# Performance work log

Hardware: AMD Instinct MI355X
Metric: run time of the kernel (lower is better)

Reference implementation:

```python
import jax, jax.numpy as jnp
import numpy as np

N = 10000
E = 320000
D_IN = 256
D_HID = 256
D_OUT = 256


def setup_inputs() -> dict:
    key = jax.random.key(0)
    ks = jax.random.split(key, 6)
    x = jax.random.normal(ks[0], (N, D_IN), dtype=jnp.float32)
    edge_index = jax.random.randint(ks[1], (2, E), 0, N, dtype=jnp.int64)
    s1 = 1.0 / np.sqrt(D_IN)
    s2 = 1.0 / np.sqrt(D_HID)
    W1 = jax.random.uniform(ks[2], (D_IN, D_HID), jnp.float32, -s1, s1)
    b1 = jax.random.uniform(ks[3], (D_HID,), jnp.float32, -s1, s1)
    W2 = jax.random.uniform(ks[4], (D_HID, D_OUT), jnp.float32, -s2, s2)
    b2 = jax.random.uniform(ks[5], (D_OUT,), jnp.float32, -s2, s2)
    return {"x": x, "edge_index": edge_index, "W1": W1, "b1": b1, "W2": W2, "b2": b2}


def reference(x, edge_index, W1, b1, W2, b2):
    # GINConv with default eps=0: h_i = (1+eps)*x_i + sum_{(j->i) in E} x_j
    src = edge_index[0]
    dst = edge_index[1]
    agg = jax.ops.segment_sum(x[src], dst, num_segments=N)  # [N, D_IN]
    h = x + agg  # eps = 0
    # 2-layer MLP: Linear -> ReLU -> Linear
    h = jax.nn.relu(jnp.dot(h, W1) + b1)
    return jnp.dot(h, W2) + b2
```

## Files before the change

kernel.cpp:

```cpp
#include <hip/hip_runtime.h>

#define NN 10000
#define EE 320000
#define DD 256
#define CAP 96
#define POISON 0xAAAAAAAAu

typedef __attribute__((ext_vector_type(8))) short short8;
typedef __attribute__((ext_vector_type(4))) float f32x4;

__device__ __forceinline__ float bf_lo(unsigned u) { return __uint_as_float(u << 16); }
__device__ __forceinline__ float bf_hi(unsigned u) { return __uint_as_float(u & 0xffff0000u); }
__device__ __forceinline__ unsigned short f2bf(float f) {
    unsigned u = __float_as_uint(f);
    u += 0x7fffu + ((u >> 16) & 1u);
    return (unsigned short)(u >> 16);
}

__global__ __launch_bounds__(256) void prep_kernel(
    const float* __restrict__ x, unsigned short* __restrict__ xb,
    const float* __restrict__ W1, const float* __restrict__ W2,
    unsigned short* __restrict__ W1t, unsigned short* __restrict__ W2t,
    const int* __restrict__ src, const int* __restrict__ dst,
    int* __restrict__ counts, int* __restrict__ slots)
{
    __shared__ float tile[64][65];
    const int bid = blockIdx.x;
    const int tid = threadIdx.x;
    if (bid < 1250) {
        const int i = bid * 2048 + tid * 8;
        const float4 a = *(const float4*)(x + i);
        const float4 b = *(const float4*)(x + i + 4);
        unsigned short o[8] = {f2bf(a.x), f2bf(a.y), f2bf(a.z), f2bf(a.w),
                               f2bf(b.x), f2bf(b.y), f2bf(b.z), f2bf(b.w)};
        *(short8*)(xb + i) = *(short8*)o;
    } else if (bid < 1282) {
        int wid = bid - 1250;
        const float* W = (wid & 16) ? W2 : W1;
        unsigned short* Wt = (wid & 16) ? W2t : W1t;
        wid &= 15;
        const int k0 = (wid & 3) * 64, n0 = (wid >> 2) * 64;
        const int tx = tid & 63, ty = tid >> 6;
        for (int r = ty; r < 64; r += 4)
            tile[r][tx] = W[(size_t)(k0 + r) * 256 + n0 + tx];
        __syncthreads();
        for (int r = ty; r < 64; r += 4)
            Wt[(size_t)(n0 + r) * 256 + k0 + tx] = f2bf(tile[tx][r]);
    } else {
        const int e = (bid - 1282) * 256 + tid;
        const int d = dst[e];
        const int s = src[e];
        const unsigned rank = (unsigned)atomicAdd(&counts[d], 1) - POISON;
        if (rank < CAP) slots[d * CAP + rank] = s;
    }
}

__global__ __launch_bounds__(256) void gather_kernel(
    const unsigned short* __restrict__ xb,
    const int* __restrict__ counts,
    const int* __restrict__ slots,
    unsigned short* __restrict__ aggb)
{
    const int wave = (int)((blockIdx.x * blockDim.x + threadIdx.x) >> 6);
    const int lane = threadIdx.x & 63;
    if (wave >= NN) return;
    int deg = (int)((unsigned)counts[wave] - POISON);
    deg = min(max(deg, 0), CAP);
    const int* sl = slots + wave * CAP;
    const uint4* xv = (const uint4*)xb;

    const int half = lane >> 5;
    const int sub  = lane & 31;

    float acc[8];
    {
        const uint4 self = xv[(size_t)wave * 32 + sub];
        const unsigned w[4] = {self.x, self.y, self.z, self.w};
#pragma unroll
        for (int q = 0; q < 4; ++q) {
            acc[2 * q]     = half ? 0.f : bf_lo(w[q]);
            acc[2 * q + 1] = half ? 0.f : bf_hi(w[q]);
        }
    }

    int j = 0;
    for (; j + 7 < deg; j += 8) {
        uint4 v[4];
#pragma unroll
        for (int u = 0; u < 4; ++u)
            v[u] = xv[(size_t)sl[j + 2 * u + half] * 32 + sub];
#pragma unroll
        for (int u = 0; u < 4; ++u) {
            const unsigned w[4] = {v[u].x, v[u].y, v[u].z, v[u].w};
#pragma unroll
            for (int q = 0; q < 4; ++q) {
                acc[2 * q]     += bf_lo(w[q]);
                acc[2 * q + 1] += bf_hi(w[q]);
            }
        }
    }
    for (; j < deg; j += 2) {
        const int k = j + half;
        const bool valid = (k < deg);
        const int n = valid ? sl[k] : wave;
        uint4 v = xv[(size_t)n * 32 + sub];
        if (!valid) { v.x = 0; v.y = 0; v.z = 0; v.w = 0; }
        const unsigned w[4] = {v.x, v.y, v.z, v.w};
#pragma unroll
        for (int q = 0; q < 4; ++q) {
            acc[2 * q]     += bf_lo(w[q]);
            acc[2 * q + 1] += bf_hi(w[q]);
        }
    }

#pragma unroll
    for (int q = 0; q < 8; ++q)
        acc[q] += __shfl_xor(acc[q], 32, 64);

    if (half == 0) {
        unsigned o[4];
#pragma unroll
        for (int q = 0; q < 4; ++q)
            o[q] = (unsigned)f2bf(acc[2 * q]) | ((unsigned)f2bf(acc[2 * q + 1]) << 16);
        ((uint4*)aggb)[(size_t)wave * 32 + sub] = make_uint4(o[0], o[1], o[2], o[3]);
    }
}

__global__ __launch_bounds__(256) void mlp_kernel(
    const unsigned short* __restrict__ aggb,
    const unsigned short* __restrict__ W1t,
    const unsigned short* __restrict__ W2t,
    const float* __restrict__ b1,
    const float* __restrict__ b2,
    float* __restrict__ out, int M)
{
    __shared__ unsigned short h1[32][264];
    const int tid = threadIdx.x;
    const int wv = tid >> 6, lane = tid & 63;
    const int quad = lane >> 4, l16 = lane & 15;
    const int m0 = blockIdx.x * 32;
    const int n0 = wv * 64;

    int rowA0 = m0 + l16;       if (rowA0 > M - 1) rowA0 = M - 1;
    int rowA1 = m0 + 16 + l16;  if (rowA1 > M - 1) rowA1 = M - 1;
    const short* Ap  = (const short*)aggb;
    const short* W1p = (const short*)W1t;
    const short* W2p = (const short*)W2t;

    f32x4 acc[2][4] = {};
#pragma unroll
    for (int kk = 0; kk < 256; kk += 32) {
        const int ko = kk + quad * 8;
        const short8 a0 = *(const short8*)(Ap + (size_t)rowA0 * 256 + ko);
        const short8 a1 = *(const short8*)(Ap + (size_t)rowA1 * 256 + ko);
#pragma unroll
        for (int j = 0; j < 4; ++j) {
            const short8 b = *(const short8*)(W1p + (size_t)(n0 + j * 16 + l16) * 256 + ko);
            acc[0][j] = __builtin_amdgcn_mfma_f32_16x16x32_bf16(a0, b, acc[0][j], 0, 0, 0);
            acc[1][j] = __builtin_amdgcn_mfma_f32_16x16x32_bf16(a1, b, acc[1][j], 0, 0, 0);
        }
    }
#pragma unroll
    for (int j = 0; j < 4; ++j) {
        const int col = n0 + j * 16 + l16;
        const float bs = b1[col];
#pragma unroll
        for (int mi = 0; mi < 2; ++mi)
#pragma unroll
            for (int r = 0; r < 4; ++r) {
                const int row = mi * 16 + quad * 4 + r;
                h1[row][col] = f2bf(fmaxf(acc[mi][j][r] + bs, 0.f));
            }
    }
    __syncthreads();

    f32x4 acc2[2][4] = {};
#pragma unroll
    for (int kk = 0; kk < 256; kk += 32) {
        const int ko = kk + quad * 8;
        const short8 a0 = *(const short8*)&h1[l16][ko];
        const short8 a1 = *(const short8*)&h1[16 + l16][ko];
#pragma unroll
        for (int j = 0; j < 4; ++j) {
            const short8 b = *(const short8*)(W2p + (size_t)(n0 + j * 16 + l16) * 256 + ko);
            acc2[0][j] = __builtin_amdgcn_mfma_f32_16x16x32_bf16(a0, b, acc2[0][j], 0, 0, 0);
            acc2[1][j] = __builtin_amdgcn_mfma_f32_16x16x32_bf16(a1, b, acc2[1][j], 0, 0, 0);
        }
    }
#pragma unroll
    for (int j = 0; j < 4; ++j) {
        const int col = n0 + j * 16 + l16;
        const float bs = b2[col];
#pragma unroll
        for (int mi = 0; mi < 2; ++mi)
#pragma unroll
            for (int r = 0; r < 4; ++r) {
                const int row = m0 + mi * 16 + quad * 4 + r;
                if (row < M)
                    out[(size_t)row * 256 + col] = acc2[mi][j][r] + bs;
            }
    }
}

extern "C" void kernel_launch(void* const* d_in, const int* in_sizes, int n_in,
                              void* d_out, int out_size, void* d_ws, size_t ws_size,
                              hipStream_t stream)
{
    const float* x   = (const float*)d_in[0];
    const int*   ei  = (const int*)d_in[1];
    const float* W1  = (const float*)d_in[2];
    const float* b1  = (const float*)d_in[3];
    const float* W2  = (const float*)d_in[4];
    const float* b2  = (const float*)d_in[5];
    float* out = (float*)d_out;

    const int E = in_sizes[1] / 2;
    const int* src = ei;
    const int* dst = ei + E;

    unsigned short* xb   = (unsigned short*)d_ws;
    unsigned short* aggb = xb + (size_t)NN * DD;
    unsigned short* W1t  = aggb + (size_t)NN * DD;
    unsigned short* W2t  = W1t + 256 * 256;
    int* counts = (int*)(W2t + 256 * 256);
    int* slots  = counts + NN;

    prep_kernel<<<2532, 256, 0, stream>>>(x, xb, W1, W2, W1t, W2t,
                                          src, dst, counts, slots);
    gather_kernel<<<(NN + 3) / 4, 256, 0, stream>>>(xb, counts, slots, aggb);
    mlp_kernel<<<(NN + 31) / 32, 256, 0, stream>>>(aggb, W1t, W2t, b1, b2, out, NN);

    (void)E; (void)ws_size; (void)n_in; (void)out_size;
}
```

Baseline: 134.7 us.

## Split gather across feature quarters, use 16-bit slot indices, enlarge MLP row tile

```diff
diff --git a/kernel.cpp b/kernel.cpp
--- a/kernel.cpp
+++ b/kernel.cpp
@@ -22,7 +22,7 @@
     const float* __restrict__ W1, const float* __restrict__ W2,
     unsigned short* __restrict__ W1t, unsigned short* __restrict__ W2t,
     const int* __restrict__ src, const int* __restrict__ dst,
-    int* __restrict__ counts, int* __restrict__ slots)
+    int* __restrict__ counts, unsigned short* __restrict__ slots)
 {
     __shared__ float tile[64][65];
     const int bid = blockIdx.x;
@@ -51,78 +51,80 @@
         const int d = dst[e];
         const int s = src[e];
         const unsigned rank = (unsigned)atomicAdd(&counts[d], 1) - POISON;
-        if (rank < CAP) slots[d * CAP + rank] = s;
+        if (rank < CAP) slots[(size_t)d * CAP + rank] = (unsigned short)s;
     }
 }
 
 __global__ __launch_bounds__(256) void gather_kernel(
     const unsigned short* __restrict__ xb,
     const int* __restrict__ counts,
-    const int* __restrict__ slots,
+    const unsigned short* __restrict__ slots,
     unsigned short* __restrict__ aggb)
 {
-    const int wave = (int)((blockIdx.x * blockDim.x + threadIdx.x) >> 6);
+    const int bid = blockIdx.x;
+    const int q = bid / 2500;
+    const int node = (bid - q * 2500) * 4 + (threadIdx.x >> 6);
     const int lane = threadIdx.x & 63;
-    if (wave >= NN) return;
-    int deg = (int)((unsigned)counts[wave] - POISON);
+    const int grp = lane >> 3, sub = lane & 7;
+    const int qoff = q * 8 + sub;
+
+    int deg = (int)((unsigned)counts[node] - POISON);
     deg = min(max(deg, 0), CAP);
-    const int* sl = slots + wave * CAP;
+    const unsigned short* sl = slots + (size_t)node * CAP;
     const uint4* xv = (const uint4*)xb;
-
-    const int half = lane >> 5;
-    const int sub  = lane & 31;
 
     float acc[8];
     {
-        const uint4 self = xv[(size_t)wave * 32 + sub];
+        const uint4 self = xv[(size_t)node * 32 + qoff];
         const unsigned w[4] = {self.x, self.y, self.z, self.w};
 #pragma unroll
-        for (int q = 0; q < 4; ++q) {
-            acc[2 * q]     = half ? 0.f : bf_lo(w[q]);
-            acc[2 * q + 1] = half ? 0.f : bf_hi(w[q]);
+        for (int t = 0; t < 4; ++t) {
+            acc[2 * t]     = grp ? 0.f : bf_lo(w[t]);
+            acc[2 * t + 1] = grp ? 0.f : bf_hi(w[t]);
         }
     }
 
+#define ACC4(v) { \
+        acc[0] += bf_lo((v).x); acc[1] += bf_hi((v).x); \
+        acc[2] += bf_lo((v).y); acc[3] += bf_hi((v).y); \
+        acc[4] += bf_lo((v).z); acc[5] += bf_hi((v).z); \
+        acc[6] += bf_lo((v).w); acc[7] += bf_hi((v).w); }
+
     int j = 0;
-    for (; j + 7 < deg; j += 8) {
-        uint4 v[4];
-#pragma unroll
-        for (int u = 0; u < 4; ++u)
-            v[u] = xv[(size_t)sl[j + 2 * u + half] * 32 + sub];
-#pragma unroll
-        for (int u = 0; u < 4; ++u) {
-            const unsigned w[4] = {v[u].x, v[u].y, v[u].z, v[u].w};
-#pragma unroll
-            for (int q = 0; q < 4; ++q) {
-                acc[2 * q]     += bf_lo(w[q]);
-                acc[2 * q + 1] += bf_hi(w[q]);
-            }
-        }
-    }
-    for (; j < deg; j += 2) {
-        const int k = j + half;
-        const bool valid = (k < deg);
-        const int n = valid ? sl[k] : wave;
-        uint4 v = xv[(size_t)n * 32 + sub];
+    for (; j + 16 <= deg; j += 16) {
+        const int s0 = (int)sl[j + grp];
+        const int s1 = (int)sl[j + 8 + grp];
+        const uint4 v0 = xv[(size_t)s0 * 32 + qoff];
+        const uint4 v1 = xv[(size_t)s1 * 32 + qoff];
+        ACC4(v0); ACC4(v1);
+    }
+    for (; j + 8 <= deg; j += 8) {
+        const int s0 = (int)sl[j + grp];
+        const uint4 v0 = xv[(size_t)s0 * 32 + qoff];
+        ACC4(v0);
+    }
+    if (j < deg) {
+        const int k = j + grp;
+        const bool valid = k < deg;
+        const int s0 = valid ? (int)sl[k] : node;
+        uint4 v = xv[(size_t)s0 * 32 + qoff];
         if (!valid) { v.x = 0; v.y = 0; v.z = 0; v.w = 0; }
-        const unsigned w[4] = {v.x, v.y, v.z, v.w};
-#pragma unroll
-        for (int q = 0; q < 4; ++q) {
-            acc[2 * q]     += bf_lo(w[q]);
-            acc[2 * q + 1] += bf_hi(w[q]);
-        }
-    }
-
-#pragma unroll
-    for (int q = 0; q < 8; ++q)
-        acc[q] += __shfl_xor(acc[q], 32, 64);
-
-    if (half == 0) {
+        ACC4(v);
+    }
+#undef ACC4
+
+#pragma unroll
+    for (int m = 8; m <= 32; m <<= 1)
+#pragma unroll
+        for (int t = 0; t < 8; ++t)
+            acc[t] += __shfl_xor(acc[t], m, 64);
+
+    if (grp == 0) {
         unsigned o[4];
 #pragma unroll
-        for (int q = 0; q < 4; ++q)
-            o[q] = (unsigned)f2bf(acc[2 * q]) | ((unsigned)f2bf(acc[2 * q + 1]) << 16);
-        ((uint4*)aggb)[(size_t)wave * 32 + sub] = make_uint4(o[0], o[1], o[2], o[3]);
+        for (int t = 0; t < 4; ++t)
+            o[t] = (unsigned)f2bf(acc[2 * t]) | ((unsigned)f2bf(acc[2 * t + 1]) << 16);
+        ((uint4*)aggb)[(size_t)node * 32 + qoff] = make_uint4(o[0], o[1], o[2], o[3]);
     }
 }
 
@@ -134,30 +136,37 @@
     const float* __restrict__ b2,
     float* __restrict__ out, int M)
 {
-    __shared__ unsigned short h1[32][264];
+    __shared__ unsigned short h1[48][264];
     const int tid = threadIdx.x;
     const int wv = tid >> 6, lane = tid & 63;
     const int quad = lane >> 4, l16 = lane & 15;
-    const int m0 = blockIdx.x * 32;
+    const int m0 = blockIdx.x * 48;
     const int n0 = wv * 64;
 
-    int rowA0 = m0 + l16;       if (rowA0 > M - 1) rowA0 = M - 1;
-    int rowA1 = m0 + 16 + l16;  if (rowA1 > M - 1) rowA1 = M - 1;
+    int rows[3];
+#pragma unroll
+    for (int mi = 0; mi < 3; ++mi) {
+        int r = m0 + mi * 16 + l16;
+        rows[mi] = r < M ? r : M - 1;
+    }
     const short* Ap  = (const short*)aggb;
     const short* W1p = (const short*)W1t;
     const short* W2p = (const short*)W2t;
 
-    f32x4 acc[2][4] = {};
+    f32x4 acc[3][4] = {};
 #pragma unroll
     for (int kk = 0; kk < 256; kk += 32) {
         const int ko = kk + quad * 8;
-        const short8 a0 = *(const short8*)(Ap + (size_t)rowA0 * 256 + ko);
-        const short8 a1 = *(const short8*)(Ap + (size_t)rowA1 * 256 + ko);
+        short8 a[3];
+#pragma unroll
+        for (int mi = 0; mi < 3; ++mi)
+            a[mi] = *(const short8*)(Ap + (size_t)rows[mi] * 256 + ko);
 #pragma unroll
         for (int j = 0; j < 4; ++j) {
             const short8 b = *(const short8*)(W1p + (size_t)(n0 + j * 16 + l16) * 256 + ko);
-            acc[0][j] = __builtin_amdgcn_mfma_f32_16x16x32_bf16(a0, b, acc[0][j], 0, 0, 0);
-            acc[1][j] = __builtin_amdgcn_mfma_f32_16x16x32_bf16(a1, b, acc[1][j], 0, 0, 0);
+#pragma unroll
+            for (int mi = 0; mi < 3; ++mi)
+                acc[mi][j] = __builtin_amdgcn_mfma_f32_16x16x32_bf16(a[mi], b, acc[mi][j], 0, 0, 0);
         }
     }
 #pragma unroll
@@ -165,7 +174,7 @@
         const int col = n0 + j * 16 + l16;
         const float bs = b1[col];
 #pragma unroll
-        for (int mi = 0; mi < 2; ++mi)
+        for (int mi = 0; mi < 3; ++mi)
 #pragma unroll
             for (int r = 0; r < 4; ++r) {
                 const int row = mi * 16 + quad * 4 + r;
@@ -174,17 +183,20 @@
     }
     __syncthreads();
 
-    f32x4 acc2[2][4] = {};
+    f32x4 acc2[3][4] = {};
 #pragma unroll
     for (int kk = 0; kk < 256; kk += 32) {
         const int ko = kk + quad * 8;
-        const short8 a0 = *(const short8*)&h1[l16][ko];
-        const short8 a1 = *(const short8*)&h1[16 + l16][ko];
+        short8 a[3];
+#pragma unroll
+        for (int mi = 0; mi < 3; ++mi)
+            a[mi] = *(const short8*)&h1[mi * 16 + l16][ko];
 #pragma unroll
         for (int j = 0; j < 4; ++j) {
             const short8 b = *(const short8*)(W2p + (size_t)(n0 + j * 16 + l16) * 256 + ko);
-            acc2[0][j] = __builtin_amdgcn_mfma_f32_16x16x32_bf16(a0, b, acc2[0][j], 0, 0, 0);
-            acc2[1][j] = __builtin_amdgcn_mfma_f32_16x16x32_bf16(a1, b, acc2[1][j], 0, 0, 0);
+#pragma unroll
+            for (int mi = 0; mi < 3; ++mi)
+                acc2[mi][j] = __builtin_amdgcn_mfma_f32_16x16x32_bf16(a[mi], b, acc2[mi][j], 0, 0, 0);
         }
     }
 #pragma unroll
@@ -192,7 +204,7 @@
         const int col = n0 + j * 16 + l16;
         const float bs = b2[col];
 #pragma unroll
-        for (int mi = 0; mi < 2; ++mi)
+        for (int mi = 0; mi < 3; ++mi)
 #pragma unroll
             for (int r = 0; r < 4; ++r) {
                 const int row = m0 + mi * 16 + quad * 4 + r;
@@ -223,12 +235,12 @@
     unsigned short* W1t  = aggb + (size_t)NN * DD;
     unsigned short* W2t  = W1t + 256 * 256;
     int* counts = (int*)(W2t + 256 * 256);
-    int* slots  = counts + NN;
+    unsigned short* slots = (unsigned short*)(counts + NN);
 
     prep_kernel<<<2532, 256, 0, stream>>>(x, xb, W1, W2, W1t, W2t,
                                           src, dst, counts, slots);
-    gather_kernel<<<(NN + 3) / 4, 256, 0, stream>>>(xb, counts, slots, aggb);
-    mlp_kernel<<<(NN + 31) / 32, 256, 0, stream>>>(aggb, W1t, W2t, b1, b2, out, NN);
+    gather_kernel<<<NN, 256, 0, stream>>>(xb, counts, slots, aggb);
+    mlp_kernel<<<(NN + 47) / 48, 256, 0, stream>>>(aggb, W1t, W2t, b1, b2, out, NN);
 
     (void)E; (void)ws_size; (void)n_in; (void)out_size;
 }
```

After: 132.2 us. No clear change (-1.9%).

## Fuse neighbor gather into MLP kernel and store slot indices as 16-bit

Applied to the files above, without the earlier changes.

```diff
diff --git a/kernel.cpp b/kernel.cpp
--- a/kernel.cpp
+++ b/kernel.cpp
@@ -22,7 +22,7 @@
     const float* __restrict__ W1, const float* __restrict__ W2,
     unsigned short* __restrict__ W1t, unsigned short* __restrict__ W2t,
     const int* __restrict__ src, const int* __restrict__ dst,
-    int* __restrict__ counts, int* __restrict__ slots)
+    int* __restrict__ counts, unsigned short* __restrict__ slots)
 {
     __shared__ float tile[64][65];
     const int bid = blockIdx.x;
@@ -51,140 +51,134 @@
         const int d = dst[e];
         const int s = src[e];
         const unsigned rank = (unsigned)atomicAdd(&counts[d], 1) - POISON;
-        if (rank < CAP) slots[d * CAP + rank] = s;
-    }
-}
-
-__global__ __launch_bounds__(256) void gather_kernel(
+        if (rank < CAP) slots[(size_t)d * CAP + rank] = (unsigned short)s;
+    }
+}
+
+__global__ __launch_bounds__(512, 4) void gather_mlp_kernel(
     const unsigned short* __restrict__ xb,
     const int* __restrict__ counts,
-    const int* __restrict__ slots,
-    unsigned short* __restrict__ aggb)
-{
-    const int wave = (int)((blockIdx.x * blockDim.x + threadIdx.x) >> 6);
-    const int lane = threadIdx.x & 63;
-    if (wave >= NN) return;
-    int deg = (int)((unsigned)counts[wave] - POISON);
-    deg = min(max(deg, 0), CAP);
-    const int* sl = slots + wave * CAP;
-    const uint4* xv = (const uint4*)xb;
-
-    const int half = lane >> 5;
-    const int sub  = lane & 31;
-
-    float acc[8];
-    {
-        const uint4 self = xv[(size_t)wave * 32 + sub];
-        const unsigned w[4] = {self.x, self.y, self.z, self.w};
-#pragma unroll
-        for (int q = 0; q < 4; ++q) {
-            acc[2 * q]     = half ? 0.f : bf_lo(w[q]);
-            acc[2 * q + 1] = half ? 0.f : bf_hi(w[q]);
-        }
-    }
-
-    int j = 0;
-    for (; j + 7 < deg; j += 8) {
-        uint4 v[4];
-#pragma unroll
-        for (int u = 0; u < 4; ++u)
-            v[u] = xv[(size_t)sl[j + 2 * u + half] * 32 + sub];
-#pragma unroll
-        for (int u = 0; u < 4; ++u) {
-            const unsigned w[4] = {v[u].x, v[u].y, v[u].z, v[u].w};
-#pragma unroll
-            for (int q = 0; q < 4; ++q) {
-                acc[2 * q]     += bf_lo(w[q]);
-                acc[2 * q + 1] += bf_hi(w[q]);
-            }
-        }
-    }
-    for (; j < deg; j += 2) {
-        const int k = j + half;
-        const bool valid = (k < deg);
-        const int n = valid ? sl[k] : wave;
-        uint4 v = xv[(size_t)n * 32 + sub];
-        if (!valid) { v.x = 0; v.y = 0; v.z = 0; v.w = 0; }
-        const unsigned w[4] = {v.x, v.y, v.z, v.w};
-#pragma unroll
-        for (int q = 0; q < 4; ++q) {
-            acc[2 * q]     += bf_lo(w[q]);
-            acc[2 * q + 1] += bf_hi(w[q]);
-        }
-    }
-
-#pragma unroll
-    for (int q = 0; q < 8; ++q)
-        acc[q] += __shfl_xor(acc[q], 32, 64);
-
-    if (half == 0) {
-        unsigned o[4];
-#pragma unroll
-        for (int q = 0; q < 4; ++q)
-            o[q] = (unsigned)f2bf(acc[2 * q]) | ((unsigned)f2bf(acc[2 * q + 1]) << 16);
-        ((uint4*)aggb)[(size_t)wave * 32 + sub] = make_uint4(o[0], o[1], o[2], o[3]);
-    }
-}
-
-__global__ __launch_bounds__(256) void mlp_kernel(
-    const unsigned short* __restrict__ aggb,
+    const unsigned short* __restrict__ slots,
     const unsigned short* __restrict__ W1t,
     const unsigned short* __restrict__ W2t,
     const float* __restrict__ b1,
     const float* __restrict__ b2,
     float* __restrict__ out, int M)
 {
-    __shared__ unsigned short h1[32][264];
+    __shared__ unsigned short buf[32][264];
     const int tid = threadIdx.x;
-    const int wv = tid >> 6, lane = tid & 63;
+    const int wave = tid >> 6, lane = tid & 63;
+    const int m0 = blockIdx.x * 32;
+
+    {
+        const int half = lane >> 5;
+        const int sub  = lane & 31;
+        const uint4* xv = (const uint4*)xb;
+
+        for (int rr = 0; rr < 4; ++rr) {
+            const int r = wave * 4 + rr;
+            int node = m0 + r; if (node > M - 1) node = M - 1;
+            int deg = (int)((unsigned)counts[node] - POISON);
+            deg = min(max(deg, 0), CAP);
+            const unsigned short* sl = slots + (size_t)node * CAP;
+
+            float acc[8];
+            {
+                const uint4 self = xv[(size_t)node * 32 + sub];
+                const unsigned w[4] = {self.x, self.y, self.z, self.w};
+#pragma unroll
+                for (int q = 0; q < 4; ++q) {
+                    acc[2 * q]     = half ? 0.f : bf_lo(w[q]);
+                    acc[2 * q + 1] = half ? 0.f : bf_hi(w[q]);
+                }
+            }
+
+            int j = 0;
+            for (; j + 7 < deg; j += 8) {
+                uint4 v[4];
+#pragma unroll
+                for (int u = 0; u < 4; ++u)
+                    v[u] = xv[(size_t)sl[j + 2 * u + half] * 32 + sub];
+#pragma unroll
+                for (int u = 0; u < 4; ++u) {
+                    const unsigned w[4] = {v[u].x, v[u].y, v[u].z, v[u].w};
+#pragma unroll
+                    for (int q = 0; q < 4; ++q) {
+                        acc[2 * q]     += bf_lo(w[q]);
+                        acc[2 * q + 1] += bf_hi(w[q]);
+                    }
+                }
+            }
+            for (; j < deg; j += 2) {
+                const int k = j + half;
+                const bool valid = (k < deg);
+                const int n = valid ? (int)sl[k] : node;
+                uint4 v = xv[(size_t)n * 32 + sub];
+                if (!valid) { v.x = 0; v.y = 0; v.z = 0; v.w = 0; }
+                const unsigned w[4] = {v.x, v.y, v.z, v.w};
+#pragma unroll
+                for (int q = 0; q < 4; ++q) {
+                    acc[2 * q]     += bf_lo(w[q]);
+                    acc[2 * q + 1] += bf_hi(w[q]);
+                }
+            }
+
+#pragma unroll
+            for (int q = 0; q < 8; ++q)
+                acc[q] += __shfl_xor(acc[q], 32, 64);
+
+            if (half == 0) {
+                unsigned o[4];
+#pragma unroll
+                for (int q = 0; q < 4; ++q)
+                    o[q] = (unsigned)f2bf(acc[2 * q]) |
+                           ((unsigned)f2bf(acc[2 * q + 1]) << 16);
+                *(uint4*)&buf[r][sub * 8] = make_uint4(o[0], o[1], o[2], o[3]);
+            }
+        }
+    }
+    __syncthreads();
+
+    const int wv2 = wave >> 2;
+    const int wn  = wave & 3;
     const int quad = lane >> 4, l16 = lane & 15;
-    const int m0 = blockIdx.x * 32;
-    const int n0 = wv * 64;
-
-    int rowA0 = m0 + l16;       if (rowA0 > M - 1) rowA0 = M - 1;
-    int rowA1 = m0 + 16 + l16;  if (rowA1 > M - 1) rowA1 = M - 1;
-    const short* Ap  = (const short*)aggb;
+    const int n0 = wn * 64;
     const short* W1p = (const short*)W1t;
     const short* W2p = (const short*)W2t;
 
-    f32x4 acc[2][4] = {};
+    f32x4 acc[4] = {};
 #pragma unroll
     for (int kk = 0; kk < 256; kk += 32) {
         const int ko = kk + quad * 8;
-        const short8 a0 = *(const short8*)(Ap + (size_t)rowA0 * 256 + ko);
-        const short8 a1 = *(const short8*)(Ap + (size_t)rowA1 * 256 + ko);
+        const short8 a = *(const short8*)&buf[wv2 * 16 + l16][ko];
 #pragma unroll
         for (int j = 0; j < 4; ++j) {
             const short8 b = *(const short8*)(W1p + (size_t)(n0 + j * 16 + l16) * 256 + ko);
-            acc[0][j] = __builtin_amdgcn_mfma_f32_16x16x32_bf16(a0, b, acc[0][j], 0, 0, 0);
-            acc[1][j] = __builtin_amdgcn_mfma_f32_16x16x32_bf16(a1, b, acc[1][j], 0, 0, 0);
-        }
-    }
+            acc[j] = __builtin_amdgcn_mfma_f32_16x16x32_bf16(a, b, acc[j], 0, 0, 0);
+        }
+    }
+    __syncthreads();
 #pragma unroll
     for (int j = 0; j < 4; ++j) {
         const int col = n0 + j * 16 + l16;
         const float bs = b1[col];
 #pragma unroll
-        for (int mi = 0; mi < 2; ++mi)
-#pragma unroll
-            for (int r = 0; r < 4; ++r) {
-                const int row = mi * 16 + quad * 4 + r;
-                h1[row][col] = f2bf(fmaxf(acc[mi][j][r] + bs, 0.f));
-            }
+        for (int r = 0; r < 4; ++r) {
+            const int row = wv2 * 16 + quad * 4 + r;
+            buf[row][col] = f2bf(fmaxf(acc[j][r] + bs, 0.f));
+        }
     }
     __syncthreads();
 
-    f32x4 acc2[2][4] = {};
+    f32x4 acc2[4] = {};
 #pragma unroll
     for (int kk = 0; kk < 256; kk += 32) {
         const int ko = kk + quad * 8;
-        const short8 a0 = *(const short8*)&h1[l16][ko];
-        const short8 a1 = *(const short8*)&h1[16 + l16][ko];
+        const short8 a = *(const short8*)&buf[wv2 * 16 + l16][ko];
 #pragma unroll
         for (int j = 0; j < 4; ++j) {
             const short8 b = *(const short8*)(W2p + (size_t)(n0 + j * 16 + l16) * 256 + ko);
-            acc2[0][j] = __builtin_amdgcn_mfma_f32_16x16x32_bf16(a0, b, acc2[0][j], 0, 0, 0);
-            acc2[1][j] = __builtin_amdgcn_mfma_f32_16x16x32_bf16(a1, b, acc2[1][j], 0, 0, 0);
+            acc2[j] = __builtin_amdgcn_mfma_f32_16x16x32_bf16(a, b, acc2[j], 0, 0, 0);
         }
     }
 #pragma unroll
@@ -192,13 +186,11 @@
         const int col = n0 + j * 16 + l16;
         const float bs = b2[col];
 #pragma unroll
-        for (int mi = 0; mi < 2; ++mi)
-#pragma unroll
-            for (int r = 0; r < 4; ++r) {
-                const int row = m0 + mi * 16 + quad * 4 + r;
-                if (row < M)
-                    out[(size_t)row * 256 + col] = acc2[mi][j][r] + bs;
-            }
+        for (int r = 0; r < 4; ++r) {
+            const int row = m0 + wv2 * 16 + quad * 4 + r;
+            if (row < M)
+                out[(size_t)row * 256 + col] = acc2[j][r] + bs;
+        }
     }
 }
 
@@ -219,16 +211,15 @@
     const int* dst = ei + E;
 
     unsigned short* xb   = (unsigned short*)d_ws;
-    unsigned short* aggb = xb + (size_t)NN * DD;
-    unsigned short* W1t  = aggb + (size_t)NN * DD;
+    unsigned short* W1t  = xb + (size_t)NN * DD;
     unsigned short* W2t  = W1t + 256 * 256;
     int* counts = (int*)(W2t + 256 * 256);
-    int* slots  = counts + NN;
+    unsigned short* slots = (unsigned short*)(counts + NN);
 
     prep_kernel<<<2532, 256, 0, stream>>>(x, xb, W1, W2, W1t, W2t,
                                           src, dst, counts, slots);
-    gather_kernel<<<(NN + 3) / 4, 256, 0, stream>>>(xb, counts, slots, aggb);
-    mlp_kernel<<<(NN + 31) / 32, 256, 0, stream>>>(aggb, W1t, W2t, b1, b2, out, NN);
+    gather_mlp_kernel<<<(NN + 31) / 32, 512, 0, stream>>>(xb, counts, slots,
+                                                          W1t, W2t, b1, b2, out, NN);
 
     (void)E; (void)ws_size; (void)n_in; (void)out_size;
 }
```

Result: slower. 145.8 us (+8.2%).
